# Kernel optimization log

Hardware: AMD Instinct MI355X
Metric: run time of the kernel (lower is better)

## Reference

```python
import jax, jax.numpy as jnp
import numpy as np

B, S, D, H, L, FF, V = 2, 1024, 1024, 16, 4, 2048, 32000
DK = D // H
EPS = 1e-5  # torch LayerNorm default


def _pos_enc(n, d):
    # matches torch PositionalEncoding: pe[pos, 2i]=sin, pe[pos, 2i+1]=cos
    pos = jnp.arange(n, dtype=jnp.float32)[:, None]
    div = jnp.exp(jnp.arange(0, d, 2, dtype=jnp.float32) * (-jnp.log(10000.0) / d))
    pe = jnp.zeros((n, d), dtype=jnp.float32)
    pe = pe.at[:, 0::2].set(jnp.sin(pos * div))
    pe = pe.at[:, 1::2].set(jnp.cos(pos * div))
    return pe


def setup_inputs() -> dict:
    key = jax.random.key(0)
    ks = jax.random.split(key, 12)
    s = 0.02
    return {
        "tokens": jax.random.randint(ks[0], (B, S), 0, V, dtype=jnp.int32),
        "emb": jax.random.normal(ks[1], (V, D), jnp.float32) * s,
        "Wq": jax.random.normal(ks[2], (L, D, D), jnp.float32) * s,
        "bq": jnp.zeros((L, D), jnp.float32),
        "Wk": jax.random.normal(ks[3], (L, D, D), jnp.float32) * s,
        "bk": jnp.zeros((L, D), jnp.float32),
        "Wv": jax.random.normal(ks[4], (L, D, D), jnp.float32) * s,
        "bv": jnp.zeros((L, D), jnp.float32),
        "Wo": jax.random.normal(ks[5], (L, D, D), jnp.float32) * s,
        "bo": jnp.zeros((L, D), jnp.float32),
        "W1": jax.random.normal(ks[6], (L, D, FF), jnp.float32) * s,
        "b1": jnp.zeros((L, FF), jnp.float32),
        "W2": jax.random.normal(ks[7], (L, FF, D), jnp.float32) * s,
        "b2": jnp.zeros((L, D), jnp.float32),
        "gamma": jnp.ones((L, D), jnp.float32),
        "beta": jnp.zeros((L, D), jnp.float32),
    }


def _layernorm(x, g, b):
    mu = jnp.mean(x, axis=-1, keepdims=True)
    var = jnp.mean(jnp.square(x - mu), axis=-1, keepdims=True)
    return (x - mu) * jax.lax.rsqrt(var + EPS) * g + b


def _encoder_layer(x, p):
    Wq, bq, Wk, bk, Wv, bv, Wo, bo, W1, b1, W2, b2, g, be = p
    # naive MHA: explicit QK^T / softmax / AV, materializing [B,H,S,S]
    q = (x @ Wq + bq).reshape(B, S, H, DK).transpose(0, 2, 1, 3)
    k = (x @ Wk + bk).reshape(B, S, H, DK).transpose(0, 2, 1, 3)
    v = (x @ Wv + bv).reshape(B, S, H, DK).transpose(0, 2, 1, 3)
    scores = jnp.einsum("bhqd,bhkd->bhqk", q, k) / jnp.sqrt(jnp.float32(DK))
    attn = jax.nn.softmax(scores, axis=-1)
    o = jnp.einsum("bhqk,bhkd->bhqd", attn, v)
    o = o.transpose(0, 2, 1, 3).reshape(B, S, D) @ Wo + bo
    # NOTE: same LayerNorm params used twice, as in the original module
    x = _layernorm(x + o, g, be)
    f = jax.nn.relu(x @ W1 + b1) @ W2 + b2
    x = _layernorm(x + f, g, be)
    return x, None


def reference(tokens, emb, Wq, bq, Wk, bk, Wv, bv, Wo, bo, W1, b1, W2, b2, gamma, beta):
    x = emb[tokens]  # [B,S,D]
    # faithful to the original bug: pe[:x.size(0)] indexes the BATCH dim,
    # pe slice has shape [B,1,D] and broadcasts over the sequence dim
    x = x + _pos_enc(B, D)[:, None, :]
    params = (Wq, bq, Wk, bk, Wv, bv, Wo, bo, W1, b1, W2, b2, gamma, beta)
    x, _ = jax.lax.scan(_encoder_layer, x, params)
    return x
```

## Files before the change

kernel.cpp:

```cpp
#include <hip/hip_runtime.h>
#include <cstdint>
#include <cstddef>

#define Bx 2
#define Sx 1024
#define Dx 1024
#define Hx 16
#define Lx 4
#define FFx 2048
#define DKx 64
#define Mx (Bx * Sx)

typedef __attribute__((ext_vector_type(4))) float f32x4;
typedef __attribute__((ext_vector_type(8))) __bf16 bf16x8;
typedef __attribute__((ext_vector_type(4))) __bf16 bf16x4;
typedef __attribute__((ext_vector_type(2))) __bf16 bf16x2;

__global__ void embed_kernel(const int* __restrict__ tokens,
                             const float* __restrict__ emb,
                             float* __restrict__ x, __bf16* __restrict__ xb) {
  size_t i = (size_t)blockIdx.x * blockDim.x + threadIdx.x;
  if (i >= (size_t)Mx * Dx / 2) return;
  int p = (int)(i % (Dx / 2));
  size_t bs = i / (Dx / 2);
  int b = (int)(bs >> 10);
  int tok = tokens[bs];
  float arg = (float)b * expf((float)(2 * p) * (-logf(10000.0f) / (float)Dx));
  float sv, cv;
  __sincosf(arg, &sv, &cv);
  const float2 e = ((const float2*)(emb + (size_t)tok * Dx))[p];
  float2 o;
  o.x = e.x + sv;
  o.y = e.y + cv;
  ((float2*)x)[i] = o;
  bf16x2 ob;
  ob[0] = (__bf16)o.x;
  ob[1] = (__bf16)o.y;
  ((bf16x2*)xb)[i] = ob;
}

__global__ void transpose_to_bf16(const float* __restrict__ W, __bf16* __restrict__ Wt,
                                  int K, int N, size_t sstride, size_t dstride) {
  __shared__ float tile[32][33];
  const float* Ws = W + blockIdx.z * sstride;
  __bf16* Wd = Wt + blockIdx.z * dstride;
  int tx = threadIdx.x, ty = threadIdx.y;
  int n0 = blockIdx.x * 32, k0 = blockIdx.y * 32;
#pragma unroll
  for (int i = 0; i < 4; ++i)
    tile[ty + 8 * i][tx] = Ws[(size_t)(k0 + ty + 8 * i) * N + n0 + tx];
  __syncthreads();
#pragma unroll
  for (int i = 0; i < 4; ++i)
    Wd[(size_t)(n0 + ty + 8 * i) * K + k0 + tx] = (__bf16)tile[tx][ty + 8 * i];
}

__global__ void concat3_kernel(const float* __restrict__ a, const float* __restrict__ b,
                               const float* __restrict__ c, float* __restrict__ out) {
  int i = blockIdx.x * 256 + threadIdx.x;
  int l = i / 3072, j = i % 3072;
  float v = (j < 1024) ? a[l * 1024 + j]
                       : ((j < 2048) ? b[l * 1024 + j - 1024] : c[l * 1024 + j - 2048]);
  out[i] = v;
}

__device__ __forceinline__ void gld_lds16(const void* g, void* l) {
  __builtin_amdgcn_global_load_lds(
      (const __attribute__((address_space(1))) void*)(uintptr_t)g,
      (__attribute__((address_space(3))) void*)(uintptr_t)l, 16, 0, 0);
}

template <int TM, int TN, bool RELU, typename OutT, bool VOUT = false>
__global__ __launch_bounds__(256) void gemm_bt(const __bf16* __restrict__ A,
                                               const __bf16* __restrict__ Bt,
                                               const float* __restrict__ bias,
                                               OutT* __restrict__ C0,
                                               float* __restrict__ C1,
                                               __bf16* __restrict__ VT,
                                               int Kstep, int Kld, int ldc) {
  static_assert((TM + TN) == 192, "NCH fixed at 12");
  __shared__ __align__(16) __bf16 lds[(TM + TN) * 32];
  const int t = threadIdx.x;
  const int w = t >> 6, lane = t & 63;
  const int quad = lane >> 4, l16 = lane & 15;
  const int m0 = blockIdx.y * TM, n0 = blockIdx.x * TN;
  const int lr = lane >> 2, lc = (lane & 3) * 8;
  const int koff = blockIdx.z * Kstep;

  f32x4 acc[2][4] = {};

  const int WR = (TN == 128) ? (w >> 1) * (TM / 2) : w * (TM / 4);
  const int WC = (TN == 128) ? (w & 1) * 64 : 0;
  const __bf16* Abase = A + (size_t)m0 * Kld + koff;
  const __bf16* Bbase = Bt + (size_t)n0 * Kld + koff;

  for (int k0 = 0; k0 < Kstep; k0 += 32) {
    __syncthreads();
#pragma unroll
    for (int c = 0; c < 3; ++c) {
      const int ch = c * 4 + w;
      const int r = ch * 16 + lr;
      const __bf16* g = (r < TM) ? (Abase + (size_t)r * Kld + k0 + lc)
                                 : (Bbase + (size_t)(r - TM) * Kld + k0 + lc);
      gld_lds16(g, (void*)(lds + ch * 512));
    }
    __syncthreads();
    bf16x8 af[2], bfr[4];
#pragma unroll
    for (int i = 0; i < 2; ++i)
      af[i] = *(const bf16x8*)&lds[(WR + i * 16 + l16) * 32 + quad * 8];
#pragma unroll
    for (int j = 0; j < 4; ++j)
      bfr[j] = *(const bf16x8*)&lds[(TM + WC + j * 16 + l16) * 32 + quad * 8];
#pragma unroll
    for (int i = 0; i < 2; ++i)
#pragma unroll
      for (int j = 0; j < 4; ++j)
        acc[i][j] = __builtin_amdgcn_mfma_f32_16x16x32_bf16(af[i], bfr[j], acc[i][j], 0, 0, 0);
  }

  const int col0 = n0 + WC + l16;

  if (VOUT && n0 >= 2048) {
    const int b = m0 >> 10;
    const int sbase = (m0 & 1023) + WR;
#pragma unroll
    for (int j = 0; j < 4; ++j) {
      const int n = col0 + j * 16;
      const int dk = n - 2048;
      const float bn = bias[n];
      __bf16* vrow = VT + (size_t)(b * 1024 + dk) * Sx + sbase;
#pragma unroll
      for (int i = 0; i < 2; ++i) {
        bf16x4 pk;
#pragma unroll
        for (int r = 0; r < 4; ++r) pk[r] = (__bf16)(acc[i][j][r] + bn);
        *(bf16x4*)(vrow + i * 16 + quad * 4) = pk;
      }
    }
    return;
  }

  const bool z0 = (blockIdx.z == 0);
#pragma unroll
  for (int j = 0; j < 4; ++j) {
    const int n = col0 + j * 16;
    const float bn = z0 ? bias[n] : 0.f;
#pragma unroll
    for (int i = 0; i < 2; ++i) {
#pragma unroll
      for (int r = 0; r < 4; ++r) {
        const int m = m0 + WR + i * 16 + quad * 4 + r;
        float v = acc[i][j][r] + bn;
        if (RELU) v = fmaxf(v, 0.f);
        if (z0)
          C0[(size_t)m * ldc + n] = (OutT)v;
        else
          C1[(size_t)m * ldc + n] = v;
      }
    }
  }
}

__global__ __launch_bounds__(256) void attention_mfma(const __bf16* __restrict__ QKV,
                                                      const __bf16* __restrict__ Vt,
                                                      __bf16* __restrict__ O) {
  __shared__ __align__(16) __bf16 Ks[2][64 * 72];
  __shared__ __align__(16) __bf16 Vs[2][64 * 72];
  __shared__ __align__(16) __bf16 Pl[64 * 72];

  const int t = threadIdx.x;
  const int w = t >> 6, lane = t & 63;
  const int quad = lane >> 4, l16 = lane & 15;
  const int q0 = blockIdx.x * 64;
  const int h = blockIdx.y, b = blockIdx.z;
  const size_t rowbase = (size_t)b * Sx;
  const int hoff = h * 64;

  const __bf16* qrow = QKV + (rowbase + q0 + w * 16 + l16) * 3072 + hoff;
  bf16x8 qf0 = *(const bf16x8*)(qrow + quad * 8);
  bf16x8 qf1 = *(const bf16x8*)(qrow + 32 + quad * 8);

  const __bf16* Kbase = QKV + rowbase * 3072 + 1024 + hoff;
  const __bf16* Vbase = Vt + (size_t)(b * Hx + h) * 64 * Sx;

  const int srow = t >> 2, sseg = t & 3;
  bf16x8 kp0, kp1, vp0, vp1;

  f32x4 oacc[4] = {};
  f32x4 lacc = {0.f, 0.f, 0.f, 0.f};
  const float cs = 0.125f * 1.44269504089f;

  {
    const __bf16* kr = Kbase + (size_t)srow * 3072 + sseg * 16;
    kp0 = *(const bf16x8*)kr;
    kp1 = *(const bf16x8*)(kr + 8);
    const __bf16* vr = Vbase + (size_t)srow * Sx + sseg * 16;
    vp0 = *(const bf16x8*)vr;
    vp1 = *(const bf16x8*)(vr + 8);
    *(bf16x8*)&Ks[0][srow * 72 + sseg * 16] = kp0;
    *(bf16x8*)&Ks[0][srow * 72 + sseg * 16 + 8] = kp1;
    *(bf16x8*)&Vs[0][srow * 72 + sseg * 16] = vp0;
    *(bf16x8*)&Vs[0][srow * 72 + sseg * 16 + 8] = vp1;
  }
  __syncthreads();

  for (int kt = 0; kt < Sx / 64; ++kt) {
    const int cur = kt & 1;
    if (kt < Sx / 64 - 1) {
      const int kn = (kt + 1) * 64;
      const __bf16* kr = Kbase + (size_t)(kn + srow) * 3072 + sseg * 16;
      kp0 = *(const bf16x8*)kr;
      kp1 = *(const bf16x8*)(kr + 8);
      const __bf16* vr = Vbase + (size_t)srow * Sx + kn + sseg * 16;
      vp0 = *(const bf16x8*)vr;
      vp1 = *(const bf16x8*)(vr + 8);
    }

    f32x4 s[4] = {};
#pragma unroll
    for (int j = 0; j < 4; ++j) {
      bf16x8 b0 = *(const bf16x8*)&Ks[cur][(j * 16 + l16) * 72 + quad * 8];
      bf16x8 b1 = *(const bf16x8*)&Ks[cur][(j * 16 + l16) * 72 + 32 + quad * 8];
      s[j] = __builtin_amdgcn_mfma_f32_16x16x32_bf16(qf0, b0, s[j], 0, 0, 0);
      s[j] = __builtin_amdgcn_mfma_f32_16x16x32_bf16(qf1, b1, s[j], 0, 0, 0);
    }

#pragma unroll
    for (int j = 0; j < 4; ++j) {
#pragma unroll
      for (int r = 0; r < 4; ++r) s[j][r] = __builtin_exp2f(s[j][r] * cs);
      lacc += s[j];
    }

#pragma unroll
    for (int r = 0; r < 4; ++r) {
      const int prow = (w * 16 + quad * 4 + r) * 72;
#pragma unroll
      for (int j = 0; j < 4; ++j) Pl[prow + j * 16 + l16] = (__bf16)s[j][r];
    }
    bf16x8 pa0 = *(const bf16x8*)&Pl[(w * 16 + l16) * 72 + quad * 8];
    bf16x8 pa1 = *(const bf16x8*)&Pl[(w * 16 + l16) * 72 + 32 + quad * 8];

#pragma unroll
    for (int j = 0; j < 4; ++j) {
      bf16x8 vb0 = *(const bf16x8*)&Vs[cur][(j * 16 + l16) * 72 + quad * 8];
      bf16x8 vb1 = *(const bf16x8*)&Vs[cur][(j * 16 + l16) * 72 + 32 + quad * 8];
      oacc[j] = __builtin_amdgcn_mfma_f32_16x16x32_bf16(pa0, vb0, oacc[j], 0, 0, 0);
      oacc[j] = __builtin_amdgcn_mfma_f32_16x16x32_bf16(pa1, vb1, oacc[j], 0, 0, 0);
    }

    if (kt < Sx / 64 - 1) {
      const int nxt = 1 - cur;
      *(bf16x8*)&Ks[nxt][srow * 72 + sseg * 16] = kp0;
      *(bf16x8*)&Ks[nxt][srow * 72 + sseg * 16 + 8] = kp1;
      *(bf16x8*)&Vs[nxt][srow * 72 + sseg * 16] = vp0;
      *(bf16x8*)&Vs[nxt][srow * 72 + sseg * 16 + 8] = vp1;
    }
    __syncthreads();
  }

#pragma unroll
  for (int r = 0; r < 4; ++r) {
    float lr = lacc[r];
    lr += __shfl_xor(lr, 1);
    lr += __shfl_xor(lr, 2);
    lr += __shfl_xor(lr, 4);
    lr += __shfl_xor(lr, 8);
    const float inv = 1.f / lr;
    const size_t orow = (rowbase + q0 + w * 16 + quad * 4 + r) * 1024 + hoff;
#pragma unroll
    for (int j = 0; j < 4; ++j) O[orow + j * 16 + l16] = (__bf16)(oacc[j][r] * inv);
  }
}

__global__ void add_ln_kernel(const float* __restrict__ x, const float* __restrict__ r0,
                              const float* __restrict__ r1,
                              const float* __restrict__ gamma, const float* __restrict__ beta,
                              float* __restrict__ out, __bf16* __restrict__ outb) {
  const int row = blockIdx.x, t = threadIdx.x;
  const int lane = t & 63, w = t >> 6;
  __shared__ float red[2][4];
  const f32x4* xr = (const f32x4*)(x + (size_t)row * Dx);
  const f32x4* a0 = (const f32x4*)(r0 + (size_t)row * Dx);
  const f32x4* a1 = (const f32x4*)(r1 + (size_t)row * Dx);
  f32x4 v = xr[t] + a0[t] + a1[t];
  float s = v[0] + v[1] + v[2] + v[3];
#pragma unroll
  for (int off = 1; off < 64; off <<= 1) s += __shfl_xor(s, off);
  if (lane == 0) red[0][w] = s;
  __syncthreads();
  const float mu = (red[0][0] + red[0][1] + red[0][2] + red[0][3]) * (1.f / Dx);
  f32x4 d = v - mu;
  float vs = d[0] * d[0] + d[1] * d[1] + d[2] * d[2] + d[3] * d[3];
#pragma unroll
  for (int off = 1; off < 64; off <<= 1) vs += __shfl_xor(vs, off);
  if (lane == 0) red[1][w] = vs;
  __syncthreads();
  const float is = rsqrtf((red[1][0] + red[1][1] + red[1][2] + red[1][3]) * (1.f / Dx) + 1e-5f);
  f32x4 g = ((const f32x4*)gamma)[t];
  f32x4 be = ((const f32x4*)beta)[t];
  f32x4 y = d * is * g + be;
  ((f32x4*)(out + (size_t)row * Dx))[t] = y;
  bf16x4 yb;
#pragma unroll
  for (int r = 0; r < 4; ++r) yb[r] = (__bf16)y[r];
  ((bf16x4*)(outb + (size_t)row * Dx))[t] = yb;
}

extern "C" void kernel_launch(void* const* d_in, const int* in_sizes, int n_in,
                              void* d_out, int out_size, void* d_ws, size_t ws_size,
                              hipStream_t stream) {
  const int* tokens = (const int*)d_in[0];
  const float* emb = (const float*)d_in[1];
  const float* Wq = (const float*)d_in[2];
  const float* bq = (const float*)d_in[3];
  const float* Wk = (const float*)d_in[4];
  const float* bk = (const float*)d_in[5];
  const float* Wv = (const float*)d_in[6];
  const float* bv = (const float*)d_in[7];
  const float* Wo = (const float*)d_in[8];
  const float* bo = (const float*)d_in[9];
  const float* W1 = (const float*)d_in[10];
  const float* b1 = (const float*)d_in[11];
  const float* W2 = (const float*)d_in[12];
  const float* b2 = (const float*)d_in[13];
  const float* gamma = (const float*)d_in[14];
  const float* beta = (const float*)d_in[15];

  const size_t M1 = 1024 * 1024;
  float* ws = (float*)d_ws;
  float* x = ws;
  float* tmp = ws + 2 * M1;
  __bf16* bfr = (__bf16*)(ws + 4 * M1);
  __bf16* xb = bfr;
  __bf16* qkvb = bfr + 2 * M1;
  __bf16* ob = bfr + 8 * M1;
  __bf16* h1b = bfr + 10 * M1;
  __bf16* Vt = bfr + 14 * M1;
  __bf16* WqkvT = bfr + 16 * M1;
  __bf16* WoT = bfr + 28 * M1;
  __bf16* W1T = bfr + 32 * M1;
  __bf16* W2T = bfr + 40 * M1;
  float* bqkv = (float*)(bfr + 48 * M1);
  float* tmp1 = (float*)qkvb;

  embed_kernel<<<((size_t)Mx * Dx / 2 + 255) / 256, 256, 0, stream>>>(tokens, emb, x, xb);

  dim3 tb(32, 8);
  transpose_to_bf16<<<dim3(32, 32, Lx), tb, 0, stream>>>(Wq, WqkvT, Dx, Dx, M1, 3 * M1);
  transpose_to_bf16<<<dim3(32, 32, Lx), tb, 0, stream>>>(Wk, WqkvT + M1, Dx, Dx, M1, 3 * M1);
  transpose_to_bf16<<<dim3(32, 32, Lx), tb, 0, stream>>>(Wv, WqkvT + 2 * M1, Dx, Dx, M1, 3 * M1);
  transpose_to_bf16<<<dim3(32, 32, Lx), tb, 0, stream>>>(Wo, WoT, Dx, Dx, M1, M1);
  transpose_to_bf16<<<dim3(64, 32, Lx), tb, 0, stream>>>(W1, W1T, Dx, FFx, 2 * M1, 2 * M1);
  transpose_to_bf16<<<dim3(32, 64, Lx), tb, 0, stream>>>(W2, W2T, FFx, Dx, 2 * M1, 2 * M1);
  concat3_kernel<<<Lx * 12, 256, 0, stream>>>(bq, bk, bv, bqkv);

  for (int l = 0; l < Lx; ++l) {
    const __bf16* WqkvT_l = WqkvT + (size_t)l * 3 * M1;
    const __bf16* WoT_l = WoT + (size_t)l * M1;
    const __bf16* W1T_l = W1T + (size_t)l * 2 * M1;
    const __bf16* W2T_l = W2T + (size_t)l * 2 * M1;
    const float* bqkv_l = bqkv + (size_t)l * 3072;
    const float* bo_l = bo + (size_t)l * Dx;
    const float* b1_l = b1 + (size_t)l * FFx;
    const float* b2_l = b2 + (size_t)l * Dx;
    const float* g_l = gamma + (size_t)l * Dx;
    const float* be_l = beta + (size_t)l * Dx;

    gemm_bt<128, 64, false, __bf16, true><<<dim3(3072 / 64, Mx / 128, 1), 256, 0, stream>>>(
        xb, WqkvT_l, bqkv_l, qkvb, nullptr, Vt, Dx, Dx, 3072);

    attention_mfma<<<dim3(Sx / 64, Hx, Bx), 256, 0, stream>>>(qkvb, Vt, ob);

    gemm_bt<64, 128, false, float><<<dim3(Dx / 128, Mx / 64, 2), 256, 0, stream>>>(
        ob, WoT_l, bo_l, tmp, tmp1, nullptr, Dx / 2, Dx, Dx);
    add_ln_kernel<<<Mx, 256, 0, stream>>>(x, tmp, tmp1, g_l, be_l, x, xb);

    gemm_bt<128, 64, true, __bf16><<<dim3(FFx / 64, Mx / 128, 1), 256, 0, stream>>>(
        xb, W1T_l, b1_l, h1b, nullptr, nullptr, Dx, Dx, FFx);
    gemm_bt<64, 128, false, float><<<dim3(Dx / 128, Mx / 64, 2), 256, 0, stream>>>(
        h1b, W2T_l, b2_l, tmp, tmp1, nullptr, FFx / 2, FFx, Dx);
    add_ln_kernel<<<Mx, 256, 0, stream>>>(x, tmp, tmp1, g_l, be_l,
                                          (l == Lx - 1) ? (float*)d_out : x, xb);
  }
}
```

Measured before the change: 806.0 us.

## Stage V-transpose through LDS, swap QK MFMA operands, merge weight transposes

```diff
diff --git a/kernel.cpp b/kernel.cpp
--- a/kernel.cpp
+++ b/kernel.cpp
@@ -55,6 +55,30 @@
     Wd[(size_t)(n0 + ty + 8 * i) * K + k0 + tx] = (__bf16)tile[tx][ty + 8 * i];
 }
 
+struct T4Args {
+  const float* s0; const float* s1; const float* s2; const float* s3;
+  __bf16* d0; __bf16* d1; __bf16* d2; __bf16* d3;
+};
+__global__ void transpose4_to_bf16(T4Args a) {
+  __shared__ float tile[32][33];
+  const int zz = blockIdx.z, l = zz >> 2, which = zz & 3;
+  const size_t M1c = (size_t)Dx * Dx;
+  const float* Ws = (which == 0 ? a.s0 : which == 1 ? a.s1 : which == 2 ? a.s2 : a.s3) + (size_t)l * M1c;
+  __bf16* Wd = (which == 0)   ? a.d0 + (size_t)l * 3 * M1c
+               : (which == 1) ? a.d1 + (size_t)l * 3 * M1c
+               : (which == 2) ? a.d2 + (size_t)l * 3 * M1c
+                              : a.d3 + (size_t)l * M1c;
+  int tx = threadIdx.x, ty = threadIdx.y;
+  int n0 = blockIdx.x * 32, k0 = blockIdx.y * 32;
+#pragma unroll
+  for (int i = 0; i < 4; ++i)
+    tile[ty + 8 * i][tx] = Ws[(size_t)(k0 + ty + 8 * i) * Dx + n0 + tx];
+  __syncthreads();
+#pragma unroll
+  for (int i = 0; i < 4; ++i)
+    Wd[(size_t)(n0 + ty + 8 * i) * Dx + k0 + tx] = (__bf16)tile[tx][ty + 8 * i];
+}
+
 __global__ void concat3_kernel(const float* __restrict__ a, const float* __restrict__ b,
                                const float* __restrict__ c, float* __restrict__ out) {
   int i = blockIdx.x * 256 + threadIdx.x;
@@ -79,7 +103,9 @@
                                                __bf16* __restrict__ VT,
                                                int Kstep, int Kld, int ldc) {
   static_assert((TM + TN) == 192, "NCH fixed at 12");
-  __shared__ __align__(16) __bf16 lds[(TM + TN) * 32];
+  static_assert(!VOUT || TN == 64, "VOUT path assumes TN=64/WC=0");
+  constexpr int LDSE = VOUT ? 64 * 136 : (TM + TN) * 32;
+  __shared__ __align__(16) __bf16 lds[LDSE];
   const int t = threadIdx.x;
   const int w = t >> 6, lane = t & 63;
   const int quad = lane >> 4, l16 = lane & 15;
@@ -122,22 +148,26 @@
   const int col0 = n0 + WC + l16;
 
   if (VOUT && n0 >= 2048) {
+    __syncthreads();
+#pragma unroll
+    for (int j = 0; j < 4; ++j) {
+      const float bn = bias[col0 + j * 16];
+      const int nl = (l16 + j * 16) * 136;
+#pragma unroll
+      for (int i = 0; i < 2; ++i)
+#pragma unroll
+        for (int r = 0; r < 4; ++r)
+          lds[nl + WR + i * 16 + quad * 4 + r] = (__bf16)(acc[i][j][r] + bn);
+    }
+    __syncthreads();
     const int b = m0 >> 10;
-    const int sbase = (m0 & 1023) + WR;
-#pragma unroll
-    for (int j = 0; j < 4; ++j) {
-      const int n = col0 + j * 16;
-      const int dk = n - 2048;
-      const float bn = bias[n];
-      __bf16* vrow = VT + (size_t)(b * 1024 + dk) * Sx + sbase;
-#pragma unroll
-      for (int i = 0; i < 2; ++i) {
-        bf16x4 pk;
-#pragma unroll
-        for (int r = 0; r < 4; ++r) pk[r] = (__bf16)(acc[i][j][r] + bn);
-        *(bf16x4*)(vrow + i * 16 + quad * 4) = pk;
-      }
-    }
+    const int sbase = m0 & 1023;
+    const int row = t >> 2, seg = t & 3;
+    __bf16* vrow = VT + (size_t)(b * 1024 + (n0 - 2048) + row) * Sx + sbase + seg * 32;
+    const __bf16* lrow = lds + row * 136 + seg * 32;
+#pragma unroll
+    for (int q = 0; q < 4; ++q)
+      *(bf16x8*)(vrow + q * 8) = *(const bf16x8*)(lrow + q * 8);
     return;
   }
 
@@ -188,7 +218,7 @@
   bf16x8 kp0, kp1, vp0, vp1;
 
   f32x4 oacc[4] = {};
-  f32x4 lacc = {0.f, 0.f, 0.f, 0.f};
+  float lsum = 0.f;
   const float cs = 0.125f * 1.44269504089f;
 
   {
@@ -222,25 +252,27 @@
     for (int j = 0; j < 4; ++j) {
       bf16x8 b0 = *(const bf16x8*)&Ks[cur][(j * 16 + l16) * 72 + quad * 8];
       bf16x8 b1 = *(const bf16x8*)&Ks[cur][(j * 16 + l16) * 72 + 32 + quad * 8];
-      s[j] = __builtin_amdgcn_mfma_f32_16x16x32_bf16(qf0, b0, s[j], 0, 0, 0);
-      s[j] = __builtin_amdgcn_mfma_f32_16x16x32_bf16(qf1, b1, s[j], 0, 0, 0);
+      s[j] = __builtin_amdgcn_mfma_f32_16x16x32_bf16(b0, qf0, s[j], 0, 0, 0);
+      s[j] = __builtin_amdgcn_mfma_f32_16x16x32_bf16(b1, qf1, s[j], 0, 0, 0);
     }
 
 #pragma unroll
     for (int j = 0; j < 4; ++j) {
 #pragma unroll
       for (int r = 0; r < 4; ++r) s[j][r] = __builtin_exp2f(s[j][r] * cs);
-      lacc += s[j];
-    }
-
-#pragma unroll
-    for (int r = 0; r < 4; ++r) {
-      const int prow = (w * 16 + quad * 4 + r) * 72;
-#pragma unroll
-      for (int j = 0; j < 4; ++j) Pl[prow + j * 16 + l16] = (__bf16)s[j][r];
-    }
-    bf16x8 pa0 = *(const bf16x8*)&Pl[(w * 16 + l16) * 72 + quad * 8];
-    bf16x8 pa1 = *(const bf16x8*)&Pl[(w * 16 + l16) * 72 + 32 + quad * 8];
+      lsum += s[j][0] + s[j][1] + s[j][2] + s[j][3];
+    }
+
+    const int prow = (w * 16 + l16) * 72;
+#pragma unroll
+    for (int j = 0; j < 4; ++j) {
+      bf16x4 pk;
+#pragma unroll
+      for (int r = 0; r < 4; ++r) pk[r] = (__bf16)s[j][r];
+      *(bf16x4*)&Pl[prow + j * 16 + quad * 4] = pk;
+    }
+    bf16x8 pa0 = *(const bf16x8*)&Pl[prow + quad * 8];
+    bf16x8 pa1 = *(const bf16x8*)&Pl[prow + 32 + quad * 8];
 
 #pragma unroll
     for (int j = 0; j < 4; ++j) {
@@ -260,17 +292,15 @@
     __syncthreads();
   }
 
+  lsum += __shfl_xor(lsum, 16);
+  lsum += __shfl_xor(lsum, 32);
+  const float inv = 1.f / lsum;
 #pragma unroll
   for (int r = 0; r < 4; ++r) {
-    float lr = lacc[r];
-    lr += __shfl_xor(lr, 1);
-    lr += __shfl_xor(lr, 2);
-    lr += __shfl_xor(lr, 4);
-    lr += __shfl_xor(lr, 8);
-    const float inv = 1.f / lr;
+    const float invr = __shfl(inv, quad * 4 + r);
     const size_t orow = (rowbase + q0 + w * 16 + quad * 4 + r) * 1024 + hoff;
 #pragma unroll
-    for (int j = 0; j < 4; ++j) O[orow + j * 16 + l16] = (__bf16)(oacc[j][r] * inv);
+    for (int j = 0; j < 4; ++j) O[orow + j * 16 + l16] = (__bf16)(oacc[j][r] * invr);
   }
 }
 
@@ -348,10 +378,8 @@
   embed_kernel<<<((size_t)Mx * Dx / 2 + 255) / 256, 256, 0, stream>>>(tokens, emb, x, xb);
 
   dim3 tb(32, 8);
-  transpose_to_bf16<<<dim3(32, 32, Lx), tb, 0, stream>>>(Wq, WqkvT, Dx, Dx, M1, 3 * M1);
-  transpose_to_bf16<<<dim3(32, 32, Lx), tb, 0, stream>>>(Wk, WqkvT + M1, Dx, Dx, M1, 3 * M1);
-  transpose_to_bf16<<<dim3(32, 32, Lx), tb, 0, stream>>>(Wv, WqkvT + 2 * M1, Dx, Dx, M1, 3 * M1);
-  transpose_to_bf16<<<dim3(32, 32, Lx), tb, 0, stream>>>(Wo, WoT, Dx, Dx, M1, M1);
+  T4Args t4{Wq, Wk, Wv, Wo, WqkvT, WqkvT + M1, WqkvT + 2 * M1, WoT};
+  transpose4_to_bf16<<<dim3(32, 32, 4 * Lx), tb, 0, stream>>>(t4);
   transpose_to_bf16<<<dim3(64, 32, Lx), tb, 0, stream>>>(W1, W1T, Dx, FFx, 2 * M1, 2 * M1);
   transpose_to_bf16<<<dim3(32, 64, Lx), tb, 0, stream>>>(W2, W2T, FFx, Dx, 2 * M1, 2 * M1);
   concat3_kernel<<<Lx * 12, 256, 0, stream>>>(bq, bk, bv, bqkv);
```

Measured after the change: 793.3 us. Within noise of the previous version (-1.6%).
